# Optimization experiments

Hardware: AMD Instinct MI355X
Metric: run time of the kernel (lower is better)

## Reference

```python
import jax, jax.numpy as jnp
import numpy as np

T, B, H = 2048, 64, 256   # time, batch, hidden/input/memory size
A = 256                   # attention_size
IN = H + H                # cell input size = input_size + memory_size = 512
NEG = -1e12


def setup_inputs() -> dict:
    key = jax.random.key(0)
    ks = jax.random.split(key, 12)
    s = lambda k, shape, fan: jax.random.normal(k, shape, jnp.float32) / np.sqrt(fan)
    inp = {
        "input": jax.random.normal(ks[0], (B, H), jnp.float32),
        "memory": jax.random.normal(ks[1], (T, B, H), jnp.float32),
        "memory_mask": jax.random.bernoulli(ks[2], 0.9, (T, B)),
        "state": jax.random.normal(ks[3], (B, H), jnp.float32),
        # attention MLP: Linear(input+state+memory -> A, no bias), Tanh, Linear(A -> 1, no bias)
        "W_a1": s(ks[4], (H + H + H, A), H * 3),
        "w_a2": s(ks[5], (A,), A),
        # gate: Linear(IN -> IN, no bias) + sigmoid
        "W_gate": s(ks[6], (IN, IN), IN),
        # GRUCell params (torch layout: [3H, in], gates order r,z,n)
        "W_ih": s(ks[7], (3 * H, IN), IN),
        "W_hh": s(ks[8], (3 * H, H), H),
        "b_ih": jnp.zeros((3 * H,), jnp.float32),
        "b_hh": jnp.zeros((3 * H,), jnp.float32),
    }
    return inp


def reference(input, memory, memory_mask, state, W_a1, w_a2, W_gate, W_ih, W_hh, b_ih, b_hh):
    # --- additive attention: tanh(W1 @ [input, state, memory]) @ w2 ---
    # split W_a1 by the concat layout [input | state | memory]
    qs = jnp.concatenate([input, state], axis=-1) @ W_a1[: 2 * H]      # [B, A]
    mp = jnp.einsum("tbh,ha->tba", memory, W_a1[2 * H :])               # [T, B, A]
    logits = jnp.tanh(qs[None] + mp) @ w_a2                              # [T, B]
    logits = jnp.where(memory_mask, logits, NEG)
    scores = jax.nn.softmax(logits, axis=0)                              # [T, B]
    attn_vec = jnp.einsum("tb,tbh->bh", scores, memory)                  # [B, H]

    # --- gate ---
    new_input = jnp.concatenate([input, attn_vec], axis=-1)              # [B, 2H]
    gated = new_input * jax.nn.sigmoid(new_input @ W_gate)

    # --- GRU cell (torch semantics, gates r, z, n) ---
    gi = gated @ W_ih.T + b_ih                                           # [B, 3H]
    gh = state @ W_hh.T + b_hh                                           # [B, 3H]
    i_r, i_z, i_n = jnp.split(gi, 3, axis=-1)
    h_r, h_z, h_n = jnp.split(gh, 3, axis=-1)
    r = jax.nn.sigmoid(i_r + h_r)
    z = jax.nn.sigmoid(i_z + h_z)
    n = jnp.tanh(i_n + r * h_n)
    return (1.0 - z) * n + z * state                                     # [B, H]
```

## Files before the change

kernel.cpp:

```cpp
#include <hip/hip_runtime.h>
#include <hip/hip_bf16.h>

#define B_DIM 64
#define H_DIM 256
#define NCHG 8
#define CHUNKS 4
#define TCH 64

typedef __attribute__((ext_vector_type(8))) short short8;
typedef __attribute__((ext_vector_type(4))) float f32x4;

__device__ __forceinline__ unsigned short bfbits(float f) {
    __hip_bfloat16 h = __float2bfloat16(f);
    unsigned short u;
    __builtin_memcpy(&u, &h, 2);
    return u;
}
__device__ __forceinline__ float fexp(float x) {
    float r;
    asm("v_exp_f32 %0, %1" : "=v"(r) : "v"(x * 1.4426950408889634f));
    return r;
}
__device__ __forceinline__ float ftanh(float x) {
    float e, r;
    asm("v_exp_f32 %0, %1" : "=v"(e) : "v"(x * 2.8853900817779268f));
    asm("v_rcp_f32 %0, %1" : "=v"(r) : "v"(e + 1.0f));
    return 1.0f - 2.0f * r;
}
__device__ __forceinline__ float fsigmoid(float x) {
    float e, r;
    asm("v_exp_f32 %0, %1" : "=v"(e) : "v"(x * -1.4426950408889634f));
    asm("v_rcp_f32 %0, %1" : "=v"(r) : "v"(e + 1.0f));
    return r;
}
__device__ __forceinline__ void lds_barrier() {
    asm volatile("s_waitcnt lgkmcnt(0)" ::: "memory");
    __builtin_amdgcn_s_barrier();
    __builtin_amdgcn_sched_barrier(0);
}

__global__ void prep_qs_kernel(const float* __restrict__ W_a1,
                               const float* __restrict__ input,
                               const float* __restrict__ state,
                               unsigned short* __restrict__ WmT,
                               float* __restrict__ qs) {
    __shared__ float cat[512];
    int bid = blockIdx.x, tid = threadIdx.x;
    if (bid < 256) {
        WmT[tid * 256 + bid] = bfbits(W_a1[(512 + bid) * 256 + tid]);
    } else {
        int b = bid - 256;
        cat[tid] = input[b * 256 + tid];
        cat[256 + tid] = state[b * 256 + tid];
        __syncthreads();
        int a = tid;
        float s0 = 0.f, s1 = 0.f, s2 = 0.f, s3 = 0.f;
        #pragma unroll 4
        for (int k = 0; k < 512; k += 4) {
            s0 += cat[k]     * W_a1[(k)     * 256 + a];
            s1 += cat[k + 1] * W_a1[(k + 1) * 256 + a];
            s2 += cat[k + 2] * W_a1[(k + 2) * 256 + a];
            s3 += cat[k + 3] * W_a1[(k + 3) * 256 + a];
        }
        qs[b * 256 + a] = (s0 + s1) + (s2 + s3);
    }
}

__global__ __launch_bounds__(512, 2) void attn_kernel(
    const float* __restrict__ memory, const int* __restrict__ mask,
    const unsigned short* __restrict__ WmT,
    const float* __restrict__ qs, const float* __restrict__ w_a2,
    float* __restrict__ part_l, float* __restrict__ part_acc)
{
    extern __shared__ char smem[];
    unsigned short* slab0 = (unsigned short*)smem;
    unsigned short* slab1 = (unsigned short*)(smem + 32768);
    float* lpart = (float*)(smem + 65536);
    int*   maskL = (int*)(smem + 65536 + 2048);

    int b = blockIdx.x, g = blockIdx.y;
    int tid = threadIdx.x;
    int lane = tid & 63, w = tid >> 6;
    int lr = lane & 15, lh = lane >> 4;
    int tbase = g * (CHUNKS * TCH);
    const float* mbase = memory + (size_t)tbase * (B_DIM * H_DIM) + b * H_DIM;

    int wa0 = w * 32;
    short8 areg[8][2];
    #pragma unroll
    for (int kk = 0; kk < 8; ++kk)
        #pragma unroll
        for (int mf = 0; mf < 2; ++mf)
            areg[kk][mf] = *(const short8*)(WmT + (wa0 + mf * 16 + lr) * 256 + kk * 32 + lh * 8);

    float qv[2][4], wv[2][4];
    #pragma unroll
    for (int mf = 0; mf < 2; ++mf)
        #pragma unroll
        for (int r = 0; r < 4; ++r) {
            int a = wa0 + mf * 16 + lh * 4 + r;
            qv[mf][r] = qs[b * 256 + a];
            wv[mf][r] = w_a2[a];
        }

    if (tid < CHUNKS * TCH) maskL[tid] = mask[(tbase + tid) * B_DIM + b];

    int wby = (lane * 8) ^ (w << 4);

    float4 ld[8];
#define ISSUE(q)                                                               \
    _Pragma("unroll") for (int i = 0; i < 8; ++i)                              \
        ld[i] = *((const float4*)(mbase + (size_t)((q) * TCH + i * 8 + w) *    \
                                  (B_DIM * H_DIM)) + lane);
#define WRITE(sl)                                                              \
    _Pragma("unroll") for (int i = 0; i < 8; ++i) {                            \
        ushort4 o;                                                             \
        o.x = bfbits(ld[i].x); o.y = bfbits(ld[i].y);                          \
        o.z = bfbits(ld[i].z); o.w = bfbits(ld[i].w);                          \
        *(ushort4*)((char*)(sl) + (i * 8 + w) * 512 + wby) = o;                \
    }

    ISSUE(0)
    WRITE(slab0)

    float a8[8] = {0.f, 0.f, 0.f, 0.f, 0.f, 0.f, 0.f, 0.f};
    float l_acc = 0.f;
    int slice4 = ((lane >> 5) + 2 * w) * 4;
    int hpvb = (lane & 31) * 16;

    for (int s = 0; s < CHUNKS; ++s) {
        const char* cur = (const char*)((s & 1) ? slab1 : slab0);
        char* nxt = (char*)((s & 1) ? slab0 : slab1);

        lds_barrier();

        if (s + 1 < CHUNKS) { ISSUE(s + 1) }

        f32x4 acc[2][4];
        #pragma unroll
        for (int mf = 0; mf < 2; ++mf)
            #pragma unroll
            for (int nf = 0; nf < 4; ++nf)
                acc[mf][nf] = (f32x4){0.f, 0.f, 0.f, 0.f};
        #pragma unroll
        for (int kk = 0; kk < 8; ++kk) {
            int kbyte = kk * 64 + lh * 16;
            #pragma unroll
            for (int nf = 0; nf < 4; ++nf) {
                int t = nf * 16 + lr;
                int sw = kbyte ^ ((t & 7) << 4);
                short8 bfr = *(const short8*)(cur + t * 512 + sw);
                acc[0][nf] = __builtin_amdgcn_mfma_f32_16x16x32_bf16(areg[kk][0], bfr, acc[0][nf], 0, 0, 0);
                acc[1][nf] = __builtin_amdgcn_mfma_f32_16x16x32_bf16(areg[kk][1], bfr, acc[1][nf], 0, 0, 0);
            }
        }

        #pragma unroll
        for (int nf = 0; nf < 4; ++nf) {
            float sv = 0.f;
            #pragma unroll
            for (int mf = 0; mf < 2; ++mf)
                #pragma unroll
                for (int r = 0; r < 4; ++r)
                    sv += wv[mf][r] * ftanh(qv[mf][r] + acc[mf][nf][r]);
            sv += __shfl_xor(sv, 16);
            sv += __shfl_xor(sv, 32);
            if (lh == 0) lpart[w * 64 + nf * 16 + lr] = sv;
        }
        lds_barrier();

        float lg = 0.f;
        #pragma unroll
        for (int ww = 0; ww < 8; ++ww) lg += lpart[ww * 64 + lane];
        float pself = maskL[s * 64 + lane] ? fexp(lg) : 0.f;
        if (w == 0) l_acc += pself;

        #pragma unroll
        for (int tt = 0; tt < 4; ++tt) {
            int tl = slice4 + tt;
            float pt = __shfl(pself, tl);
            int swb = hpvb ^ ((tl & 7) << 4);
            uint4 u = *(const uint4*)(cur + tl * 512 + swb);
            a8[0] += pt * __uint_as_float(u.x << 16);
            a8[1] += pt * __uint_as_float(u.x & 0xFFFF0000u);
            a8[2] += pt * __uint_as_float(u.y << 16);
            a8[3] += pt * __uint_as_float(u.y & 0xFFFF0000u);
            a8[4] += pt * __uint_as_float(u.z << 16);
            a8[5] += pt * __uint_as_float(u.z & 0xFFFF0000u);
            a8[6] += pt * __uint_as_float(u.w << 16);
            a8[7] += pt * __uint_as_float(u.w & 0xFFFF0000u);
        }

        if (s + 1 < CHUNKS) { WRITE(nxt) }
    }
#undef ISSUE
#undef WRITE

    __syncthreads();
    float* acc2 = (float*)smem;
    int oct = lane & 31, slice = 2 * w + (lane >> 5), h0 = oct * 8;
    *(float4*)(&acc2[slice * 256 + h0])     = (float4){a8[0], a8[1], a8[2], a8[3]};
    *(float4*)(&acc2[slice * 256 + h0 + 4]) = (float4){a8[4], a8[5], a8[6], a8[7]};
    __syncthreads();
    int pidx = g * B_DIM + b;
    if (tid < 256) {
        float ssum = 0.f;
        #pragma unroll
        for (int sl = 0; sl < 16; ++sl) ssum += acc2[sl * 256 + tid];
        part_acc[(size_t)pidx * 256 + tid] = ssum;
    }
    if (w == 0) {
        #pragma unroll
        for (int d = 1; d < 64; d <<= 1) l_acc += __shfl_xor(l_acc, d);
        if (lane == 0) part_l[pidx] = l_acc;
    }
}

__global__ void mergegate_kernel(const float* __restrict__ part_l,
                                 const float* __restrict__ part_acc,
                                 const float* __restrict__ input,
                                 const float* __restrict__ W_gate,
                                 float* __restrict__ gated) {
    __shared__ float ni[512];
    int b = blockIdx.x, tid = threadIdx.x;
    if (tid >= 256) {
        int k = tid - 256;
        ni[k] = input[b * 256 + k];
    } else {
        int h = tid;
        float L = 0.f, s = 0.f;
        #pragma unroll
        for (int c = 0; c < NCHG; ++c) {
            L += part_l[c * 64 + b];
            s += part_acc[(size_t)(c * 64 + b) * 256 + h];
        }
        ni[256 + h] = s / L;
    }
    __syncthreads();
    int j = tid;
    float s0 = 0.f, s1 = 0.f, s2 = 0.f, s3 = 0.f;
    #pragma unroll 4
    for (int k = 0; k < 512; k += 4) {
        s0 += ni[k]     * W_gate[(k)     * 512 + j];
        s1 += ni[k + 1] * W_gate[(k + 1) * 512 + j];
        s2 += ni[k + 2] * W_gate[(k + 2) * 512 + j];
        s3 += ni[k + 3] * W_gate[(k + 3) * 512 + j];
    }
    float s = (s0 + s1) + (s2 + s3);
    gated[b * 512 + j] = ni[j] * fsigmoid(s);
}

__global__ __launch_bounds__(768) void gru_kernel(
    const float* __restrict__ gated, const float* __restrict__ state,
    const float* __restrict__ W_ih, const float* __restrict__ W_hh,
    const float* __restrict__ b_ih, const float* __restrict__ b_hh,
    float* __restrict__ out) {
    __shared__ float ld_g[4][512];
    __shared__ float ld_s[4][256];
    __shared__ float xi[3][16][4];
    __shared__ float xh[3][16][4];
    int ht = blockIdx.x & 15, bt = blockIdx.x >> 4;
    int tid = threadIdx.x;
    #pragma unroll
    for (int i = 0; i < 3; ++i) {
        int idx = i * 768 + tid;
        if (idx < 2048) ld_g[idx >> 9][idx & 511] = gated[(bt * 4 + (idx >> 9)) * 512 + (idx & 511)];
    }
    #pragma unroll
    for (int i = 0; i < 2; ++i) {
        int idx = i * 768 + tid;
        if (idx < 1024) ld_s[idx >> 8][idx & 255] = state[(bt * 4 + (idx >> 8)) * 256 + (idx & 255)];
    }

    int gid = tid >> 4, lk = tid & 15;
    int gate = gid >> 4, hl = gid & 15;
    int j = gate * 256 + ht * 16 + hl;

    float4 wi[8], wh[4];
    #pragma unroll
    for (int it = 0; it < 8; ++it)
        wi[it] = *(const float4*)(W_ih + (size_t)j * 512 + it * 64 + lk * 4);
    #pragma unroll
    for (int it = 0; it < 4; ++it)
        wh[it] = *(const float4*)(W_hh + (size_t)j * 256 + it * 64 + lk * 4);
    float bi = b_ih[j], bh = b_hh[j];
    __syncthreads();

    #pragma unroll
    for (int bb = 0; bb < 4; ++bb) {
        float g0 = 0.f, g1 = 0.f;
        #pragma unroll
        for (int it = 0; it < 8; ++it) {
            float4 gv = *(const float4*)(&ld_g[bb][it * 64 + lk * 4]);
            g0 += wi[it].x * gv.x + wi[it].z * gv.z;
            g1 += wi[it].y * gv.y + wi[it].w * gv.w;
        }
        float h0 = 0.f, h1 = 0.f;
        #pragma unroll
        for (int it = 0; it < 4; ++it) {
            float4 sv = *(const float4*)(&ld_s[bb][it * 64 + lk * 4]);
            h0 += wh[it].x * sv.x + wh[it].z * sv.z;
            h1 += wh[it].y * sv.y + wh[it].w * sv.w;
        }
        float gi_ = g0 + g1, gh_ = h0 + h1;
        #pragma unroll
        for (int m = 1; m < 16; m <<= 1) {
            gi_ += __shfl_xor(gi_, m);
            gh_ += __shfl_xor(gh_, m);
        }
        if (lk == 0) { xi[gate][hl][bb] = gi_ + bi; xh[gate][hl][bb] = gh_ + bh; }
    }
    __syncthreads();
    if (tid < 64) {
        int bb = tid >> 4, hl2 = tid & 15;
        float ir = xi[0][hl2][bb], hr = xh[0][hl2][bb];
        float iz = xi[1][hl2][bb], hz = xh[1][hl2][bb];
        float in_ = xi[2][hl2][bb], hn = xh[2][hl2][bb];
        float r = fsigmoid(ir + hr);
        float z = fsigmoid(iz + hz);
        float n = ftanh(in_ + r * hn);
        out[(bt * 4 + bb) * 256 + ht * 16 + hl2] =
            (1.f - z) * n + z * ld_s[bb][ht * 16 + hl2];
    }
}

extern "C" void kernel_launch(void* const* d_in, const int* in_sizes, int n_in,
                              void* d_out, int out_size, void* d_ws, size_t ws_size,
                              hipStream_t stream) {
    const float* input  = (const float*)d_in[0];
    const float* memory = (const float*)d_in[1];
    const int*   mask   = (const int*)d_in[2];
    const float* state  = (const float*)d_in[3];
    const float* W_a1   = (const float*)d_in[4];
    const float* w_a2   = (const float*)d_in[5];
    const float* W_gate = (const float*)d_in[6];
    const float* W_ih   = (const float*)d_in[7];
    const float* W_hh   = (const float*)d_in[8];
    const float* b_ih   = (const float*)d_in[9];
    const float* b_hh   = (const float*)d_in[10];
    float* out = (float*)d_out;

    char* ws = (char*)d_ws;
    unsigned short* WmT = (unsigned short*)(ws + 0);
    float* qs       = (float*)(ws + 131072);
    float* gated    = (float*)(ws + 196608);
    float* part_l   = (float*)(ws + 327680);
    float* part_acc = (float*)(ws + 335872);

    prep_qs_kernel<<<320, 256, 0, stream>>>(W_a1, input, state, WmT, qs);

    (void)hipFuncSetAttribute((const void*)attn_kernel,
                              hipFuncAttributeMaxDynamicSharedMemorySize, 68608);
    attn_kernel<<<dim3(B_DIM, NCHG), 512, 68608, stream>>>(
        memory, mask, WmT, qs, w_a2, part_l, part_acc);

    mergegate_kernel<<<64, 512, 0, stream>>>(part_l, part_acc, input, W_gate, gated);
    gru_kernel<<<256, 768, 0, stream>>>(gated, state, W_ih, W_hh, b_ih, b_hh, out);
}
```

Measured before the change: 78.60 us.

## Fuse gate and GRU cell into a single per-batch tail kernel

Merges the merge/gate kernel and the GRU kernel into one kernel with one block per batch row, keeping the gated vector and state in shared memory and dropping one launch and the global gated buffer. Each block now computes all 768 GRU gate rows itself, reading the full W_ih and W_hh matrices per block. This trades launch overhead and an intermediate round trip for much more weight traffic per block and fewer blocks doing the GRU matvec.

```diff
diff --git a/kernel.cpp b/kernel.cpp
--- a/kernel.cpp
+++ b/kernel.cpp
@@ -216,16 +216,24 @@
     }
 }
 
-__global__ void mergegate_kernel(const float* __restrict__ part_l,
-                                 const float* __restrict__ part_acc,
-                                 const float* __restrict__ input,
-                                 const float* __restrict__ W_gate,
-                                 float* __restrict__ gated) {
+__global__ __launch_bounds__(512) void tail_kernel(
+    const float* __restrict__ part_l, const float* __restrict__ part_acc,
+    const float* __restrict__ input,  const float* __restrict__ state,
+    const float* __restrict__ W_gate,
+    const float* __restrict__ W_ih,   const float* __restrict__ W_hh,
+    const float* __restrict__ b_ih,   const float* __restrict__ b_hh,
+    float* __restrict__ out) {
     __shared__ float ni[512];
+    __shared__ float gL[512];
+    __shared__ float st[256];
+    __shared__ float xi[768];
+    __shared__ float xh[768];
     int b = blockIdx.x, tid = threadIdx.x;
+
     if (tid >= 256) {
         int k = tid - 256;
         ni[k] = input[b * 256 + k];
+        st[k] = state[b * 256 + k];
     } else {
         int h = tid;
         float L = 0.f, s = 0.f;
@@ -237,90 +245,63 @@
         ni[256 + h] = s / L;
     }
     __syncthreads();
-    int j = tid;
-    float s0 = 0.f, s1 = 0.f, s2 = 0.f, s3 = 0.f;
-    #pragma unroll 4
-    for (int k = 0; k < 512; k += 4) {
-        s0 += ni[k]     * W_gate[(k)     * 512 + j];
-        s1 += ni[k + 1] * W_gate[(k + 1) * 512 + j];
-        s2 += ni[k + 2] * W_gate[(k + 2) * 512 + j];
-        s3 += ni[k + 3] * W_gate[(k + 3) * 512 + j];
-    }
-    float s = (s0 + s1) + (s2 + s3);
-    gated[b * 512 + j] = ni[j] * fsigmoid(s);
-}
-
-__global__ __launch_bounds__(768) void gru_kernel(
-    const float* __restrict__ gated, const float* __restrict__ state,
-    const float* __restrict__ W_ih, const float* __restrict__ W_hh,
-    const float* __restrict__ b_ih, const float* __restrict__ b_hh,
-    float* __restrict__ out) {
-    __shared__ float ld_g[4][512];
-    __shared__ float ld_s[4][256];
-    __shared__ float xi[3][16][4];
-    __shared__ float xh[3][16][4];
-    int ht = blockIdx.x & 15, bt = blockIdx.x >> 4;
-    int tid = threadIdx.x;
-    #pragma unroll
-    for (int i = 0; i < 3; ++i) {
-        int idx = i * 768 + tid;
-        if (idx < 2048) ld_g[idx >> 9][idx & 511] = gated[(bt * 4 + (idx >> 9)) * 512 + (idx & 511)];
-    }
-    #pragma unroll
-    for (int i = 0; i < 2; ++i) {
-        int idx = i * 768 + tid;
-        if (idx < 1024) ld_s[idx >> 8][idx & 255] = state[(bt * 4 + (idx >> 8)) * 256 + (idx & 255)];
-    }
-
-    int gid = tid >> 4, lk = tid & 15;
-    int gate = gid >> 4, hl = gid & 15;
-    int j = gate * 256 + ht * 16 + hl;
-
-    float4 wi[8], wh[4];
-    #pragma unroll
-    for (int it = 0; it < 8; ++it)
-        wi[it] = *(const float4*)(W_ih + (size_t)j * 512 + it * 64 + lk * 4);
-    #pragma unroll
-    for (int it = 0; it < 4; ++it)
-        wh[it] = *(const float4*)(W_hh + (size_t)j * 256 + it * 64 + lk * 4);
-    float bi = b_ih[j], bh = b_hh[j];
-    __syncthreads();
-
-    #pragma unroll
-    for (int bb = 0; bb < 4; ++bb) {
-        float g0 = 0.f, g1 = 0.f;
-        #pragma unroll
-        for (int it = 0; it < 8; ++it) {
-            float4 gv = *(const float4*)(&ld_g[bb][it * 64 + lk * 4]);
-            g0 += wi[it].x * gv.x + wi[it].z * gv.z;
-            g1 += wi[it].y * gv.y + wi[it].w * gv.w;
-        }
-        float h0 = 0.f, h1 = 0.f;
-        #pragma unroll
-        for (int it = 0; it < 4; ++it) {
-            float4 sv = *(const float4*)(&ld_s[bb][it * 64 + lk * 4]);
-            h0 += wh[it].x * sv.x + wh[it].z * sv.z;
-            h1 += wh[it].y * sv.y + wh[it].w * sv.w;
-        }
-        float gi_ = g0 + g1, gh_ = h0 + h1;
-        #pragma unroll
-        for (int m = 1; m < 16; m <<= 1) {
-            gi_ += __shfl_xor(gi_, m);
-            gh_ += __shfl_xor(gh_, m);
-        }
-        if (lk == 0) { xi[gate][hl][bb] = gi_ + bi; xh[gate][hl][bb] = gh_ + bh; }
-    }
-    __syncthreads();
-    if (tid < 64) {
-        int bb = tid >> 4, hl2 = tid & 15;
-        float ir = xi[0][hl2][bb], hr = xh[0][hl2][bb];
-        float iz = xi[1][hl2][bb], hz = xh[1][hl2][bb];
-        float in_ = xi[2][hl2][bb], hn = xh[2][hl2][bb];
-        float r = fsigmoid(ir + hr);
-        float z = fsigmoid(iz + hz);
-        float n = ftanh(in_ + r * hn);
-        out[(bt * 4 + bb) * 256 + ht * 16 + hl2] =
-            (1.f - z) * n + z * ld_s[bb][ht * 16 + hl2];
+
+    {
+        int j = tid;
+        float s0 = 0.f, s1 = 0.f, s2 = 0.f, s3 = 0.f;
+        #pragma unroll 4
+        for (int k = 0; k < 512; k += 4) {
+            s0 += ni[k]     * W_gate[(k)     * 512 + j];
+            s1 += ni[k + 1] * W_gate[(k + 1) * 512 + j];
+            s2 += ni[k + 2] * W_gate[(k + 2) * 512 + j];
+            s3 += ni[k + 3] * W_gate[(k + 3) * 512 + j];
+        }
+        float s = (s0 + s1) + (s2 + s3);
+        gL[j] = ni[j] * fsigmoid(s);
+    }
+    __syncthreads();
+
+    {
+        int grp = tid >> 4, lk = tid & 15;
+        const float4* gp = (const float4*)(&gL[0]);
+        const float4* sp = (const float4*)(&st[0]);
+        for (int m = 0; m < 24; ++m) {
+            int j = grp + 32 * m;
+            float si = 0.f;
+            const float4* wi = (const float4*)(W_ih + (size_t)j * 512);
+            #pragma unroll
+            for (int it = 0; it < 8; ++it) {
+                float4 wvv = wi[it * 16 + lk];
+                float4 gv = gp[it * 16 + lk];
+                si += wvv.x * gv.x + wvv.y * gv.y + wvv.z * gv.z + wvv.w * gv.w;
+            }
+            float sh = 0.f;
+            const float4* wh = (const float4*)(W_hh + (size_t)j * 256);
+            #pragma unroll
+            for (int it = 0; it < 4; ++it) {
+                float4 wvv = wh[it * 16 + lk];
+                float4 sv = sp[it * 16 + lk];
+                sh += wvv.x * sv.x + wvv.y * sv.y + wvv.z * sv.z + wvv.w * sv.w;
+            }
+            #pragma unroll
+            for (int d = 1; d < 16; d <<= 1) {
+                si += __shfl_xor(si, d);
+                sh += __shfl_xor(sh, d);
+            }
+            if (lk == 0) {
+                xi[j] = si + b_ih[j];
+                xh[j] = sh + b_hh[j];
+            }
+        }
+    }
+    __syncthreads();
+
+    if (tid < 256) {
+        int h = tid;
+        float r = fsigmoid(xi[h]       + xh[h]);
+        float z = fsigmoid(xi[256 + h] + xh[256 + h]);
+        float n = ftanh(xi[512 + h] + r * xh[512 + h]);
+        out[b * 256 + h] = (1.f - z) * n + z * st[h];
     }
 }
 
@@ -343,7 +324,6 @@
     char* ws = (char*)d_ws;
     unsigned short* WmT = (unsigned short*)(ws + 0);
     float* qs       = (float*)(ws + 131072);
-    float* gated    = (float*)(ws + 196608);
     float* part_l   = (float*)(ws + 327680);
     float* part_acc = (float*)(ws + 335872);
 
@@ -354,6 +334,6 @@
     attn_kernel<<<dim3(B_DIM, NCHG), 512, 68608, stream>>>(
         memory, mask, WmT, qs, w_a2, part_l, part_acc);
 
-    mergegate_kernel<<<64, 512, 0, stream>>>(part_l, part_acc, input, W_gate, gated);
-    gru_kernel<<<256, 768, 0, stream>>>(gated, state, W_ih, W_hh, b_ih, b_hh, out);
-}
+    tail_kernel<<<64, 512, 0, stream>>>(part_l, part_acc, input, state,
+                                        W_gate, W_ih, W_hh, b_ih, b_hh, out);
+}
```

New measurement: 110.4 us. 40.5% more time.

## Split merge and gate into separate kernels with batch-tiled gate GEMV

Applied to the files above, without the earlier changes.

Splits the fused merge+gate kernel in two. A small merge kernel writes attn_vec to workspace, and a new gate kernel is tiled over 32 output columns and 8 batch rows per block. Each W_gate element is now reused across 8 batch rows instead of being re-read once per batch, which cuts weight traffic, and the grid grows from 64 to 128 blocks. The cost is an extra kernel launch and a global round-trip for attn_vec.

```diff
diff --git a/kernel.cpp b/kernel.cpp
--- a/kernel.cpp
+++ b/kernel.cpp
@@ -216,38 +216,45 @@
     }
 }
 
-__global__ void mergegate_kernel(const float* __restrict__ part_l,
-                                 const float* __restrict__ part_acc,
-                                 const float* __restrict__ input,
-                                 const float* __restrict__ W_gate,
-                                 float* __restrict__ gated) {
-    __shared__ float ni[512];
-    int b = blockIdx.x, tid = threadIdx.x;
-    if (tid >= 256) {
-        int k = tid - 256;
-        ni[k] = input[b * 256 + k];
-    } else {
-        int h = tid;
-        float L = 0.f, s = 0.f;
-        #pragma unroll
-        for (int c = 0; c < NCHG; ++c) {
-            L += part_l[c * 64 + b];
-            s += part_acc[(size_t)(c * 64 + b) * 256 + h];
-        }
-        ni[256 + h] = s / L;
-    }
-    __syncthreads();
-    int j = tid;
+__global__ void merge_kernel(const float* __restrict__ part_l,
+                             const float* __restrict__ part_acc,
+                             float* __restrict__ attn_vec) {
+    int b = blockIdx.x, h = threadIdx.x;
+    float L = 0.f, s = 0.f;
+    #pragma unroll
+    for (int c = 0; c < NCHG; ++c) {
+        L += part_l[c * 64 + b];
+        s += part_acc[(size_t)(c * 64 + b) * 256 + h];
+    }
+    attn_vec[b * 256 + h] = s / L;
+}
+
+__global__ void gate_kernel(const float* __restrict__ input,
+                            const float* __restrict__ attn_vec,
+                            const float* __restrict__ W_gate,
+                            float* __restrict__ gated) {
+    __shared__ float ni[8][516];
+    int j0 = blockIdx.x * 32, b0 = blockIdx.y * 8;
+    int tid = threadIdx.x;
+    #pragma unroll
+    for (int i = 0; i < 16; ++i) {
+        int idx = i * 256 + tid;
+        int row = idx >> 9, k = idx & 511;
+        ni[row][k] = (k < 256) ? input[(b0 + row) * 256 + k]
+                               : attn_vec[(b0 + row) * 256 + k - 256];
+    }
+    __syncthreads();
+    int j = j0 + (tid & 31), row = tid >> 5;
     float s0 = 0.f, s1 = 0.f, s2 = 0.f, s3 = 0.f;
     #pragma unroll 4
     for (int k = 0; k < 512; k += 4) {
-        s0 += ni[k]     * W_gate[(k)     * 512 + j];
-        s1 += ni[k + 1] * W_gate[(k + 1) * 512 + j];
-        s2 += ni[k + 2] * W_gate[(k + 2) * 512 + j];
-        s3 += ni[k + 3] * W_gate[(k + 3) * 512 + j];
+        s0 += ni[row][k]     * W_gate[(k)     * 512 + j];
+        s1 += ni[row][k + 1] * W_gate[(k + 1) * 512 + j];
+        s2 += ni[row][k + 2] * W_gate[(k + 2) * 512 + j];
+        s3 += ni[row][k + 3] * W_gate[(k + 3) * 512 + j];
     }
     float s = (s0 + s1) + (s2 + s3);
-    gated[b * 512 + j] = ni[j] * fsigmoid(s);
+    gated[(b0 + row) * 512 + j] = ni[row][j] * fsigmoid(s);
 }
 
 __global__ __launch_bounds__(768) void gru_kernel(
@@ -346,6 +353,7 @@
     float* gated    = (float*)(ws + 196608);
     float* part_l   = (float*)(ws + 327680);
     float* part_acc = (float*)(ws + 335872);
+    float* attn_vec = (float*)(ws + 860160);
 
     prep_qs_kernel<<<320, 256, 0, stream>>>(W_a1, input, state, WmT, qs);
 
@@ -354,6 +362,7 @@
     attn_kernel<<<dim3(B_DIM, NCHG), 512, 68608, stream>>>(
         memory, mask, WmT, qs, w_a2, part_l, part_acc);
 
-    mergegate_kernel<<<64, 512, 0, stream>>>(part_l, part_acc, input, W_gate, gated);
+    merge_kernel<<<64, 256, 0, stream>>>(part_l, part_acc, attn_vec);
+    gate_kernel<<<dim3(16, 8), 256, 0, stream>>>(input, attn_vec, W_gate, gated);
     gru_kernel<<<256, 768, 0, stream>>>(gated, state, W_ih, W_hh, b_ih, b_hh, out);
 }
```

After: 83.95 us. +6.8%, slower.
